# Optimization experiments

Hardware: AMD Instinct MI355X
Metric: run time of the kernel (lower is better)

## Reference

```python
import jax, jax.numpy as jnp
import numpy as np

B, D, H, N, K, C = 1024, 256, 512, 100000, 96, 10


def setup_inputs() -> dict:
    key = jax.random.key(0)
    ks = jax.random.split(key, 16)
    s = 0.02
    return {
        "x": jax.random.normal(ks[0], (B, D), jnp.float32),
        "candidate_x": jax.random.normal(ks[1], (N, D), jnp.float32),
        "candidate_labels": jax.random.randint(ks[2], (N,), 0, C, jnp.int32),
        "W_enc": jax.random.normal(ks[3], (D, H), jnp.float32) * s,
        "b_enc": jnp.zeros((H,), jnp.float32),
        "W_key": jax.random.normal(ks[4], (H, H), jnp.float32) * s,
        "b_key": jnp.zeros((H,), jnp.float32),
        "W_val": jax.random.normal(ks[5], (H, H), jnp.float32) * s,
        "b_val": jnp.zeros((H,), jnp.float32),
        "E_label": jax.random.normal(ks[6], (C, H), jnp.float32) * s,
        "W_t1": jax.random.normal(ks[7], (H, H), jnp.float32) * s,
        "b_t1": jnp.zeros((H,), jnp.float32),
        "W_t2": jax.random.normal(ks[8], (H, H), jnp.float32) * s,
    }


def reference(x, candidate_x, candidate_labels, W_enc, b_enc, W_key, b_key,
              W_val, b_val, E_label, W_t1, b_t1, W_t2):
    # Encode queries and candidates
    x_enc = x @ W_enc + b_enc                       # [B, H]
    cand_enc = candidate_x @ W_enc + b_enc          # [N, H]
    x_key = x_enc @ W_key + b_key                   # [B, H]
    cand_keys = cand_enc @ W_key + b_key            # [N, H]

    # Negative euclidean distance via GEMM expansion (compute-efficient cdist)
    q2 = jnp.sum(x_key * x_key, axis=-1, keepdims=True)        # [B, 1]
    c2 = jnp.sum(cand_keys * cand_keys, axis=-1)               # [N]
    d2 = q2 + c2[None, :] - 2.0 * (x_key @ cand_keys.T)        # [B, N]
    sim = -jnp.sqrt(jnp.maximum(d2, 0.0))                      # [B, N]

    # Top-k retrieval
    top_sims, top_idx = jax.lax.top_k(sim, K)                  # [B, K]

    cand_vals = cand_enc @ W_val + b_val                       # [N, H]
    label_emb = E_label[candidate_labels]                      # [N, H]

    ctx_keys = cand_keys[top_idx]                              # [B, K, H]
    ctx_labels = label_emb[top_idx]                            # [B, K, H]
    _ = cand_vals[top_idx]  # gathered values (unused by the original math)

    # Attention over retrieved context (softmax of top-k similarities)
    attn = jax.nn.softmax(top_sims, axis=1)                    # [B, K]

    # Correction MLP T (dropout is identity in eval mode)
    diff = x_key[:, None, :] - ctx_keys                        # [B, K, H]
    t_out = jax.nn.relu(diff @ W_t1 + b_t1) @ W_t2             # [B, K, H]

    ctx_vec = jnp.sum(attn[..., None] * (ctx_labels + t_out), axis=1)  # [B, H]
    return x_enc + ctx_vec
```

## Files before the change

### kernel.cpp

```cpp
#include <hip/hip_runtime.h>
#include <cfloat>
#include <cmath>

#define B_ 1024
#define D_ 256
#define H_ 512
#define N_ 100000
#define K_ 96
#define C_ 10
#define SAMP 8192
#define CAPC 4096
#define RCAP 15

typedef __attribute__((ext_vector_type(8))) short bf16x8;
typedef __attribute__((ext_vector_type(4))) float f32x4;

__device__ __forceinline__ float bf2f(ushort h) {
    union { unsigned u; float f; } v; v.u = ((unsigned)h) << 16; return v.f;
}
__device__ __forceinline__ ushort f2bf(float f) {
    union { float f; unsigned u; } v; v.f = f;
    unsigned u = v.u;
    unsigned r = (u + 0x7fffu + ((u >> 16) & 1u)) >> 16;
    return (ushort)r;
}
__device__ __forceinline__ unsigned f2key(float f) {
    unsigned u = __float_as_uint(f);
    return (u & 0x80000000u) ? ~u : (u | 0x80000000u);
}
__device__ __forceinline__ float d2_of(float acc, float q2, float c2) {
    return fmaxf(fmaf(-2.f, acc, q2 + c2), 0.f);
}

#define GLDS(g, l)                                                            \
    __builtin_amdgcn_global_load_lds(                                         \
        (const __attribute__((address_space(1))) void*)(g),                   \
        (__attribute__((address_space(3))) void*)(l), 16, 0, 0)

template <int RELU>
__global__ __launch_bounds__(256) void gemm_nn(const float* __restrict__ A,
                                               const float* __restrict__ Bm,
                                               const float* __restrict__ bias,
                                               float* __restrict__ Cm,
                                               int M, int N, int Kd) {
    __shared__ float sA[16][68];
    __shared__ float sB[16][64];
    const int t  = threadIdx.x;
    const int tx = t & 15, ty = t >> 4;
    const int m0 = blockIdx.y * 64;
    const int n0 = blockIdx.x * 64;
    const int lr = t >> 2;
    const int lk = (t & 3) << 2;
    const int bk = t >> 4;
    const int bn = (t & 15) << 2;

    float acc[4][4] = {};
    for (int k0 = 0; k0 < Kd; k0 += 16) {
        float4 av = make_float4(0.f, 0.f, 0.f, 0.f);
        if (m0 + lr < M)
            av = *(const float4*)(A + (size_t)(m0 + lr) * Kd + k0 + lk);
        sA[lk + 0][lr] = av.x; sA[lk + 1][lr] = av.y;
        sA[lk + 2][lr] = av.z; sA[lk + 3][lr] = av.w;
        float4 bv = *(const float4*)(Bm + (size_t)(k0 + bk) * N + n0 + bn);
        *(float4*)&sB[bk][bn] = bv;
        __syncthreads();
#pragma unroll
        for (int kk = 0; kk < 16; ++kk) {
            float4 a4 = *(const float4*)&sA[kk][ty << 2];
            float4 b4 = *(const float4*)&sB[kk][tx << 2];
            float ar[4] = {a4.x, a4.y, a4.z, a4.w};
            float br[4] = {b4.x, b4.y, b4.z, b4.w};
#pragma unroll
            for (int i = 0; i < 4; ++i)
#pragma unroll
                for (int j = 0; j < 4; ++j)
                    acc[i][j] = fmaf(ar[i], br[j], acc[i][j]);
        }
        __syncthreads();
    }
#pragma unroll
    for (int i = 0; i < 4; ++i) {
        int row = m0 + (ty << 2) + i;
        if (row < M) {
            int col = n0 + (tx << 2);
            float b0 = 0.f, b1 = 0.f, b2 = 0.f, b3 = 0.f;
            if (bias) { b0 = bias[col]; b1 = bias[col + 1]; b2 = bias[col + 2]; b3 = bias[col + 3]; }
            float4 o;
            o.x = acc[i][0] + b0; o.y = acc[i][1] + b1;
            o.z = acc[i][2] + b2; o.w = acc[i][3] + b3;
            if (RELU) {
                o.x = fmaxf(o.x, 0.f); o.y = fmaxf(o.y, 0.f);
                o.z = fmaxf(o.z, 0.f); o.w = fmaxf(o.w, 0.f);
            }
            *(float4*)(Cm + (size_t)row * N + col) = o;
        }
    }
}

template <int MODE, int SWZ>
__global__ __launch_bounds__(256) void gemm_nt(const ushort* __restrict__ A,
                                               const ushort* __restrict__ Bv,
                                               const float* __restrict__ bias,
                                               const float* __restrict__ q2v,
                                               const float* __restrict__ c2v,
                                               const float* __restrict__ thrv,
                                               float* __restrict__ candV,
                                               int* __restrict__ candI,
                                               int* __restrict__ cnt,
                                               void* __restrict__ Cout,
                                               int M, int Nlim, int K,
                                               int ldc, int nvalid, int per) {
    int m0, n0;
    if (SWZ == 0) {
        m0 = blockIdx.y * 128; n0 = blockIdx.x * 128;
    } else if (SWZ == 1) {
        int bid = blockIdx.x;
        int xcd = bid & 7, slot = bid >> 3;
        m0 = (slot & 7) * 128;
        n0 = (xcd * per + (slot >> 3)) * 128;
        if (n0 >= nvalid || m0 >= M) return;
    } else {
        int bid = blockIdx.x;
        int xcd = bid & 7, slot = bid >> 3;
        n0 = (slot & 3) * 128;
        m0 = (xcd * per + (slot >> 2)) * 128;
        if (m0 >= M) return;
    }

    __shared__ __align__(16) char smem[16896];
    ushort* sA = (ushort*)smem;
    ushort* sB = (ushort*)(smem + 8192);
    const int t = threadIdx.x;
    const int lane = t & 63, w = t >> 6;
    const int wm = w & 1, wn = w >> 1;

    f32x4 acc[4][4];
#pragma unroll
    for (int i = 0; i < 4; ++i)
#pragma unroll
        for (int j = 0; j < 4; ++j)
            acc[i][j] = (f32x4){0.f, 0.f, 0.f, 0.f};

    const int la = lane & 15, lk = lane >> 4;
    const int aoff = (wm * 64 + la) * 64 + lk * 16;
    const int boff = (wn * 64 + la) * 64 + lk * 16;
    const int r_ = t >> 2, cc_ = (t & 3);

    for (int k0 = 0; k0 < K; k0 += 32) {
#pragma unroll
        for (int q = 0; q < 2; ++q) {
            int r = r_ + q * 64;
            int ar = m0 + r; ar = (ar < M) ? ar : (M - 1);
            GLDS(A + (size_t)ar * K + k0 + cc_ * 8, (char*)sA + (q * 256 + t) * 16);
            int br = n0 + r; br = (br < Nlim) ? br : (Nlim - 1);
            GLDS(Bv + (size_t)br * K + k0 + cc_ * 8, (char*)sB + (q * 256 + t) * 16);
        }
        __syncthreads();
        bf16x8 af[4], bfr[4];
#pragma unroll
        for (int i = 0; i < 4; ++i)
            af[i] = *(const bf16x8*)((const char*)sA + aoff + i * 1024);
#pragma unroll
        for (int j = 0; j < 4; ++j)
            bfr[j] = *(const bf16x8*)((const char*)sB + boff + j * 1024);
#pragma unroll
        for (int i = 0; i < 4; ++i)
#pragma unroll
            for (int j = 0; j < 4; ++j)
                acc[i][j] = __builtin_amdgcn_mfma_f32_16x16x32_bf16(
                    af[i], bfr[j], acc[i][j], 0, 0, 0);
        __syncthreads();
    }

    const int rl = (lane >> 4) * 4, cl = lane & 15;

    if (MODE == 5) {
        float* stV = (float*)smem;
        int*   stI = (int*)(smem + 7680);
        int*   stC = (int*)(smem + 16384);
        for (int r = t; r < 128; r += 256) stC[r] = 0;
        __syncthreads();
#pragma unroll
        for (int i = 0; i < 4; ++i) {
#pragma unroll
            for (int v = 0; v < 4; ++v) {
                int rloc = wm * 64 + i * 16 + rl + v;
                int gr = m0 + rloc;
                float q2b = q2v[gr];
                float th = thrv[gr];
#pragma unroll
                for (int j = 0; j < 4; ++j) {
                    int gc = n0 + wn * 64 + j * 16 + cl;
                    if (gc < nvalid) {
                        float d2 = d2_of(acc[i][j][v], q2b, c2v[gc]);
                        if (d2 <= th) {
                            int p = atomicAdd(&stC[rloc], 1);
                            if (p < RCAP) {
                                stV[rloc * RCAP + p] = d2;
                                stI[rloc * RCAP + p] = gc;
                            }
                        }
                    }
                }
            }
        }
        __syncthreads();
        for (int r = t; r < 128; r += 256) {
            int n = stC[r]; if (n > RCAP) n = RCAP;
            if (n > 0) {
                int gr = m0 + r;
                int gb = atomicAdd(&cnt[gr], n);
                for (int q = 0; q < n; ++q) {
                    int pos = gb + q;
                    if (pos < CAPC) {
                        candV[(size_t)gr * CAPC + pos] = stV[r * RCAP + q];
                        candI[(size_t)gr * CAPC + pos] = stI[r * RCAP + q];
                    }
                }
            }
        }
        return;
    }

#pragma unroll
    for (int i = 0; i < 4; ++i) {
#pragma unroll
        for (int j = 0; j < 4; ++j) {
            int gc = n0 + wn * 64 + j * 16 + cl;
#pragma unroll
            for (int v = 0; v < 4; ++v) {
                int gr = m0 + wm * 64 + i * 16 + rl + v;
                if (gr < M && gc < nvalid) {
                    float val = acc[i][j][v];
                    if (MODE == 2) {
                        ((float*)Cout)[(size_t)gr * ldc + gc] = val;
                    } else {
                        if (MODE == 1 || MODE == 3) val += bias[gc];
                        if (MODE == 1) val = fmaxf(val, 0.f);
                        ((ushort*)Cout)[(size_t)gr * ldc + gc] = f2bf(val);
                    }
                }
            }
        }
    }
}

__global__ __launch_bounds__(256) void thr_select(const float* __restrict__ S,
                                                  int ld,
                                                  const float* __restrict__ q2v,
                                                  const float* __restrict__ c2v,
                                                  float* __restrict__ thrArr) {
    __shared__ unsigned keys[SAMP];
    __shared__ int hist[256];
    __shared__ int sel[2];
    const int b = blockIdx.x, t = threadIdx.x;
    const float q2b = q2v[b];
    for (int i = t; i < SAMP; i += 256)
        keys[i] = ~f2key(d2_of(S[(size_t)b * ld + i], q2b, c2v[i]));
    __syncthreads();
    unsigned prefix = 0, mask = 0;
    int rank = K_;
    for (int shift = 24; shift >= 0; shift -= 8) {
        hist[t & 255] = 0;
        __syncthreads();
        for (int i = t; i < SAMP; i += 256) {
            unsigned k = keys[i];
            if ((k & mask) == prefix) atomicAdd(&hist[(k >> shift) & 255], 1);
        }
        __syncthreads();
        if (t == 0) {
            int r = rank, d = 255;
            for (; d > 0; --d) { int c = hist[d]; if (r - c <= 0) break; r -= c; }
            sel[0] = d; sel[1] = (r < 1) ? 1 : r;
        }
        __syncthreads();
        prefix |= ((unsigned)sel[0]) << shift;
        rank = sel[1];
        mask |= (0xFFu << shift);
        __syncthreads();
    }
    if (t == 0) {
        unsigned key = ~prefix;
        thrArr[b] = __uint_as_float(key & 0x7FFFFFFFu);
    }
}

__global__ __launch_bounds__(256) void final_select(const float* __restrict__ candV,
                                                    const int* __restrict__ candI,
                                                    const int* __restrict__ cnt,
                                                    float* __restrict__ topV,
                                                    int* __restrict__ topI) {
    __shared__ unsigned keys[CAPC];
    __shared__ int hist[256];
    __shared__ int sel[2];
    __shared__ int poscnt, eqcnt;
    const int b = blockIdx.x, t = threadIdx.x;
    int n = cnt[b]; if (n > CAPC) n = CAPC;
    for (int i = t; i < n; i += 256)
        keys[i] = ~f2key(candV[(size_t)b * CAPC + i]);
    __syncthreads();
    unsigned prefix = 0, mask = 0;
    int rank = K_;
    for (int shift = 24; shift >= 0; shift -= 8) {
        hist[t & 255] = 0;
        __syncthreads();
        for (int i = t; i < n; i += 256) {
            unsigned k = keys[i];
            if ((k & mask) == prefix) atomicAdd(&hist[(k >> shift) & 255], 1);
        }
        __syncthreads();
        if (t == 0) {
            int r = rank, d = 255;
            for (; d > 0; --d) { int c = hist[d]; if (r - c <= 0) break; r -= c; }
            sel[0] = d; sel[1] = (r < 1) ? 1 : r;
        }
        __syncthreads();
        prefix |= ((unsigned)sel[0]) << shift;
        rank = sel[1];
        mask |= (0xFFu << shift);
        __syncthreads();
    }
    unsigned kth = prefix;
    if (t == 0) { poscnt = 0; eqcnt = 0; }
    __syncthreads();
    for (int i = t; i < n; i += 256) {
        if (keys[i] > kth) {
            int p = atomicAdd(&poscnt, 1);
            topV[b * K_ + p] = candV[(size_t)b * CAPC + i];
            topI[b * K_ + p] = candI[(size_t)b * CAPC + i];
        }
    }
    __syncthreads();
    int base = poscnt;
    for (int i = t; i < n; i += 256) {
        if (keys[i] == kth) {
            int p = atomicAdd(&eqcnt, 1);
            if (base + p < K_) {
                topV[b * K_ + base + p] = candV[(size_t)b * CAPC + i];
                topI[b * K_ + base + p] = candI[(size_t)b * CAPC + i];
            }
        }
    }
}

__global__ void init_cnt(int* cnt) {
    int i = blockIdx.x * 256 + threadIdx.x;
    if (i < B_) cnt[i] = 0;
}

__global__ void conv_f2b(const float* __restrict__ in, ushort* __restrict__ out, int n) {
    int i = (blockIdx.x * 256 + threadIdx.x) * 4;
    int stride = gridDim.x * 256 * 4;
    for (; i < n; i += stride) {
        float4 v = *(const float4*)(in + i);
        ushort4 o;
        o.x = f2bf(v.x); o.y = f2bf(v.y); o.z = f2bf(v.z); o.w = f2bf(v.w);
        *(ushort4*)(out + i) = o;
    }
}

__global__ __launch_bounds__(256) void transpose_f2b(const float* __restrict__ in,
                                                     ushort* __restrict__ out,
                                                     int R, int Cn) {
    __shared__ float tile[32][33];
    int bx = blockIdx.x * 32, by = blockIdx.y * 32;
    int tx = threadIdx.x & 31, ty = threadIdx.x >> 5;
    int x = bx + tx;
#pragma unroll
    for (int dy = 0; dy < 32; dy += 8) {
        int y = by + ty + dy;
        if (x < Cn && y < R) tile[ty + dy][tx] = in[(size_t)y * Cn + x];
    }
    __syncthreads();
    int ox = by + tx;
#pragma unroll
    for (int dy = 0; dy < 32; dy += 8) {
        int oy = bx + ty + dy;
        if (ox < R && oy < Cn) out[(size_t)oy * R + ox] = f2bf(tile[tx][ty + dy]);
    }
}

__global__ __launch_bounds__(64) void rowsq_b(const ushort* __restrict__ X,
                                              float* __restrict__ outv) {
    const int r = blockIdx.x, t = threadIdx.x;
    const ushort* p = X + (size_t)r * H_;
    ushort4 a = *(const ushort4*)(p + t * 4);
    ushort4 b = *(const ushort4*)(p + 256 + t * 4);
    float ax = bf2f(a.x), ay = bf2f(a.y), az = bf2f(a.z), aw = bf2f(a.w);
    float bx = bf2f(b.x), by = bf2f(b.y), bz = bf2f(b.z), bw = bf2f(b.w);
    float v = ax * ax + ay * ay + az * az + aw * aw +
              bx * bx + by * by + bz * bz + bw * bw;
    for (int off = 32; off > 0; off >>= 1) v += __shfl_down(v, off);
    if (t == 0) outv[r] = v;
}

__global__ void bcomb_k(const float* __restrict__ b_enc,
                        const float* __restrict__ W_key,
                        const float* __restrict__ b_key,
                        float* __restrict__ b_comb) {
    int h = blockIdx.x * 256 + threadIdx.x;
    if (h >= H_) return;
    float acc = b_key[h];
    for (int m = 0; m < H_; ++m)
        acc = fmaf(b_enc[m], W_key[(size_t)m * H_ + h], acc);
    b_comb[h] = acc;
}

__global__ __launch_bounds__(128) void softmax_k(const float* __restrict__ topVal,
                                                 float* __restrict__ attn) {
    __shared__ float red[128];
    const int b = blockIdx.x, t = threadIdx.x;
    float v = (t < K_) ? -sqrtf(topVal[b * K_ + t]) : -FLT_MAX;
    red[t] = v; __syncthreads();
    for (int s = 64; s > 0; s >>= 1) {
        if (t < s) red[t] = fmaxf(red[t], red[t + s]);
        __syncthreads();
    }
    float m = red[0]; __syncthreads();
    float e = (t < K_) ? expf(v - m) : 0.f;
    red[t] = e; __syncthreads();
    for (int s = 64; s > 0; s >>= 1) {
        if (t < s) red[t] += red[t + s];
        __syncthreads();
    }
    float ssum = red[0];
    if (t < K_) attn[b * K_ + t] = e / ssum;
}

__global__ __launch_bounds__(128) void gather_diff_b(const float* __restrict__ XK,
                                                     const ushort* __restrict__ CK,
                                                     const int* __restrict__ topI,
                                                     ushort* __restrict__ diff,
                                                     int b0) {
    const int r = blockIdx.x;
    const int b = b0 + r / K_;
    const int idx = topI[b * K_ + (r % K_)];
    const int t = threadIdx.x;
    float4 xv = *(const float4*)(XK + (size_t)b * H_ + t * 4);
    ushort4 cv = *(const ushort4*)(CK + (size_t)idx * H_ + t * 4);
    ushort4 o;
    o.x = f2bf(xv.x - bf2f(cv.x));
    o.y = f2bf(xv.y - bf2f(cv.y));
    o.z = f2bf(xv.z - bf2f(cv.z));
    o.w = f2bf(xv.w - bf2f(cv.w));
    *(ushort4*)(diff + (size_t)r * H_ + t * 4) = o;
}

__global__ __launch_bounds__(256) void wsum_h(const float* __restrict__ attn,
                                              const ushort* __restrict__ h,
                                              ushort* __restrict__ hw, int b0) {
    const int bl = blockIdx.x;
    const int b = b0 + bl;
    const int t = threadIdx.x;
    float a0 = 0.f, a1 = 0.f;
    const float* ap = attn + b * K_;
    for (int k = 0; k < K_; ++k) {
        float w = ap[k];
        const ushort* hr = h + (size_t)(bl * K_ + k) * H_;
        a0 = fmaf(w, bf2f(hr[t]), a0);
        a1 = fmaf(w, bf2f(hr[t + 256]), a1);
    }
    hw[(size_t)b * H_ + t]       = f2bf(a0);
    hw[(size_t)b * H_ + t + 256] = f2bf(a1);
}

__global__ __launch_bounds__(256) void final_out(const float* __restrict__ attn,
                                                 const int* __restrict__ topI,
                                                 const int* __restrict__ labels,
                                                 const float* __restrict__ E,
                                                 const float* __restrict__ tsum,
                                                 const float* __restrict__ xe,
                                                 float* __restrict__ out) {
    const int b = blockIdx.x, t = threadIdx.x;
    float a0 = 0.f, a1 = 0.f;
    for (int k = 0; k < K_; ++k) {
        float w = attn[b * K_ + k];
        int idx = topI[b * K_ + k];
        int lab = labels[idx];
        const float* el = E + (size_t)lab * H_;
        a0 = fmaf(w, el[t], a0);
        a1 = fmaf(w, el[t + 256], a1);
    }
    out[(size_t)b * H_ + t] =
        xe[(size_t)b * H_ + t] + a0 + tsum[(size_t)b * H_ + t];
    out[(size_t)b * H_ + t + 256] =
        xe[(size_t)b * H_ + t + 256] + a1 + tsum[(size_t)b * H_ + t + 256];
}

extern "C" void kernel_launch(void* const* d_in, const int* in_sizes, int n_in,
                              void* d_out, int out_size, void* d_ws, size_t ws_size,
                              hipStream_t stream) {
    const float* x      = (const float*)d_in[0];
    const float* cx     = (const float*)d_in[1];
    const int*   labels = (const int*)d_in[2];
    const float* W_enc  = (const float*)d_in[3];
    const float* b_enc  = (const float*)d_in[4];
    const float* W_key  = (const float*)d_in[5];
    const float* b_key  = (const float*)d_in[6];
    const float* E_label = (const float*)d_in[9];
    const float* W_t1   = (const float*)d_in[10];
    const float* b_t1   = (const float*)d_in[11];
    const float* W_t2   = (const float*)d_in[12];
    float* out = (float*)d_out;

    char* base = (char*)d_ws;
    size_t off = 0;
    auto take = [&](size_t n) -> char* {
        char* p = base + off;
        off = (off + n + 255) & ~(size_t)255;
        return p;
    };
    float*  Wc    = (float*)take((size_t)D_ * H_ * 4);
    float*  bc    = (float*)take((size_t)H_ * 4);
    ushort* WcT   = (ushort*)take((size_t)H_ * D_ * 2);
    ushort* Wt1T  = (ushort*)take((size_t)H_ * H_ * 2);
    ushort* Wt2T  = (ushort*)take((size_t)H_ * H_ * 2);
    float*  xe    = (float*)take((size_t)B_ * H_ * 4);
    float*  xk    = (float*)take((size_t)B_ * H_ * 4);
    ushort* xkb   = (ushort*)take((size_t)B_ * H_ * 2);
    float*  q2    = (float*)take((size_t)B_ * 4);
    ushort* ckb   = (ushort*)take((size_t)N_ * H_ * 2);
    float*  c2    = (float*)take((size_t)N_ * 4);
    float*  topV  = (float*)take((size_t)B_ * K_ * 4);
    int*    topI  = (int*)take((size_t)B_ * K_ * 4);
    float*  thr   = (float*)take((size_t)B_ * 4);
    float*  attn  = (float*)take((size_t)B_ * K_ * 4);
    int*    cnt   = (int*)take((size_t)B_ * 4);
    float*  candV = (float*)take((size_t)B_ * CAPC * 4);
    int*    candI = (int*)take((size_t)B_ * CAPC * 4);
    ushort* hwAll = (ushort*)take((size_t)B_ * H_ * 2);
    float*  tsum  = (float*)take((size_t)B_ * H_ * 4);
    char*   big   = base + off;
    size_t rem = (ws_size > off) ? (ws_size - off) : 0;

    ushort* cxb      = (ushort*)big;
    float*  simSmall = (float*)big;

    long long bcq = (long long)(rem / ((size_t)K_ * H_ * 2 * 2));
    if (bcq > B_) bcq = B_;
    if (bcq < 1) bcq = 1;
    int Bc = (int)bcq;

    {
        dim3 g(H_ / 64, D_ / 64);
        gemm_nn<0><<<g, 256, 0, stream>>>(W_enc, W_key, nullptr, Wc, D_, H_, H_);
        bcomb_k<<<(H_ + 255) / 256, 256, 0, stream>>>(b_enc, W_key, b_key, bc);
        dim3 gt1((H_ + 31) / 32, (D_ + 31) / 32);
        transpose_f2b<<<gt1, 256, 0, stream>>>(Wc, WcT, D_, H_);
        dim3 gt2((H_ + 31) / 32, (H_ + 31) / 32);
        transpose_f2b<<<gt2, 256, 0, stream>>>(W_t1, Wt1T, H_, H_);
        transpose_f2b<<<gt2, 256, 0, stream>>>(W_t2, Wt2T, H_, H_);
    }
    {
        dim3 gx(H_ / 64, B_ / 64);
        gemm_nn<0><<<gx, 256, 0, stream>>>(x, W_enc, b_enc, xe, B_, H_, D_);
        gemm_nn<0><<<gx, 256, 0, stream>>>(x, Wc, bc, xk, B_, H_, D_);
        conv_f2b<<<1024, 256, 0, stream>>>(xk, xkb, B_ * H_);
        conv_f2b<<<2048, 256, 0, stream>>>(cx, cxb, N_ * D_);
    }
    {
        int mt = (N_ + 127) / 128;
        int mper = (mt + 7) / 8;
        gemm_nt<3, 2><<<8 * mper * 4, 256, 0, stream>>>(
            cxb, WcT, bc, nullptr, nullptr, nullptr, nullptr, nullptr, nullptr,
            ckb, N_, H_, D_, H_, H_, mper);
    }
    rowsq_b<<<N_, 64, 0, stream>>>(ckb, c2);
    rowsq_b<<<B_, 64, 0, stream>>>(xkb, q2);

    {
        int nper = (SAMP / 128 + 7) / 8;
        gemm_nt<2, 1><<<64 * nper, 256, 0, stream>>>(
            xkb, ckb, nullptr, nullptr, nullptr, nullptr, nullptr, nullptr,
            nullptr, simSmall, B_, N_, H_, SAMP, SAMP, nper);
        thr_select<<<B_, 256, 0, stream>>>(simSmall, SAMP, q2, c2, thr);
    }
    init_cnt<<<(B_ + 255) / 256, 256, 0, stream>>>(cnt);
    {
        int NT = (N_ + 127) / 128;
        int nper = (NT + 7) / 8;
        gemm_nt<5, 1><<<64 * nper, 256, 0, stream>>>(
            xkb, ckb, nullptr, q2, c2, thr, candV, candI, cnt,
            nullptr, B_, N_, H_, 0, N_, nper);
    }
    final_select<<<B_, 256, 0, stream>>>(candV, candI, cnt, topV, topI);
    softmax_k<<<B_, 128, 0, stream>>>(topV, attn);

    ushort* diffB = (ushort*)big;
    ushort* hB = (ushort*)(big + (size_t)Bc * K_ * H_ * 2);
    for (int b0 = 0; b0 < B_; b0 += Bc) {
        int bcn = min(Bc, B_ - b0);
        int Mrows = bcn * K_;
        gather_diff_b<<<Mrows, 128, 0, stream>>>(xk, ckb, topI, diffB, b0);
        int mt4 = (Mrows + 127) / 128;
        int mper4 = (mt4 + 7) / 8;
        gemm_nt<1, 2><<<8 * mper4 * 4, 256, 0, stream>>>(
            diffB, Wt1T, b_t1, nullptr, nullptr, nullptr, nullptr, nullptr,
            nullptr, hB, Mrows, H_, H_, H_, H_, mper4);
        wsum_h<<<bcn, 256, 0, stream>>>(attn, hB, hwAll, b0);
    }
    {
        dim3 g(H_ / 128, B_ / 128);
        gemm_nt<2, 0><<<g, 256, 0, stream>>>(
            hwAll, Wt2T, nullptr, nullptr, nullptr, nullptr, nullptr, nullptr,
            nullptr, tsum, B_, H_, H_, H_, H_, 0);
    }
    final_out<<<B_, 256, 0, stream>>>(attn, topI, labels, E_label, tsum, xe, out);
}
```

Measured before the change: 968.9 us.

## Add 256x256-tile 8-wave GEMM with ping-pong LDS pipeline for large GEMMs

Introduces a new gemm256 kernel that uses 256x256 output tiles with 512 threads, double-buffered global-to-LDS staging, and interleaved MFMA/LDS-read phases with explicit barriers and priority hints. It replaces the 128-tile gemm_nt in the candidate-key projection, the fused distance/threshold-filter GEMM, and the correction-MLP first layer. Larger tiles raise arithmetic intensity and data reuse per workgroup, and the filter epilogue now stages survivors per row in a larger shared buffer before writing them out globally. The cost is higher register and LDS use (128KB shared), possible occupancy loss, and tile-quantisation waste on ragged M.

```diff
diff --git a/kernel.cpp b/kernel.cpp
--- a/kernel.cpp
+++ b/kernel.cpp
@@ -11,6 +11,7 @@
 #define SAMP 8192
 #define CAPC 4096
 #define RCAP 15
+#define RCAP2 24
 
 typedef __attribute__((ext_vector_type(8))) short bf16x8;
 typedef __attribute__((ext_vector_type(4))) float f32x4;
@@ -243,6 +244,219 @@
             }
         }
     }
+}
+
+#define FENCE() asm volatile("" ::: "memory")
+#define PBAR()                                                                \
+    { FENCE(); __builtin_amdgcn_s_barrier();                                  \
+      asm volatile("s_waitcnt lgkmcnt(0)" ::: "memory"); }
+#define PBARV4()                                                              \
+    { asm volatile("s_waitcnt vmcnt(4)" ::: "memory");                        \
+      __builtin_amdgcn_s_barrier(); FENCE(); }
+#define BAR2()                                                                \
+    { FENCE(); __builtin_amdgcn_s_barrier(); FENCE(); }
+
+template <int MODE, int MMINOR>
+__global__ __launch_bounds__(512, 2) void gemm256(
+    const ushort* __restrict__ A, const ushort* __restrict__ Bv,
+    const float* __restrict__ bias, const float* __restrict__ q2v,
+    const float* __restrict__ c2v, const float* __restrict__ thrv,
+    float* __restrict__ candV, int* __restrict__ candI, int* __restrict__ cnt,
+    void* __restrict__ Cout, int M, int Nlim, int K, int ldc, int nvalid) {
+    __shared__ __align__(16) char smem[131072];
+
+    const int nwg = gridDim.x;
+    const int MT = (M + 255) >> 8;
+    const int q8 = nwg >> 3, r8 = nwg & 7;
+    const int xcd = blockIdx.x & 7, lin = blockIdx.x >> 3;
+    const int wgid =
+        (xcd < r8 ? xcd * (q8 + 1) : r8 * (q8 + 1) + (xcd - r8) * q8) + lin;
+    int mt, nt;
+    if (MMINOR) { mt = wgid % MT; nt = wgid / MT; }
+    else        { int NT = nwg / MT; nt = wgid % NT; mt = wgid / NT; }
+    const int m0 = mt << 8, n0 = nt << 8;
+
+    const int t = threadIdx.x;
+    const int lane = t & 63, w = t >> 6;
+    const int wm = w & 1, wn = w >> 1;
+    const int la = lane & 15, lk = lane >> 4;
+    const int e7 = la & 7;
+    const int gk0 = (lk ^ e7) << 4;
+    const int gk1 = ((4 | lk) ^ e7) << 4;
+
+    char* sA = smem;
+    char* sB = smem + 65536;
+    const int rbA = wm * 16384 + la * 128;
+    const int rbB = (wn >> 1) * 16384 + ((wn & 1) * 64 + la) * 128;
+
+    const int g8   = (((t & 7) ^ ((t >> 3) & 7)) << 3);
+    const int srow = t >> 3;
+    const int sdst = t * 16;
+
+    auto stageA = [&](int kt, int buf) {
+        const ushort* p = A + kt * 64 + g8;
+        char* d = sA + buf * 32768;
+#pragma unroll
+        for (int h = 0; h < 2; ++h)
+#pragma unroll
+            for (int qq = 0; qq < 2; ++qq) {
+                int row = m0 + h * 128 + qq * 64 + srow;
+                row = (row < M) ? row : (M - 1);
+                GLDS(p + (size_t)row * K, d + h * 16384 + qq * 8192 + sdst);
+            }
+    };
+    auto stageB = [&](int kt, int buf) {
+        const ushort* p = Bv + kt * 64 + g8;
+        char* d = sB + buf * 32768;
+#pragma unroll
+        for (int h = 0; h < 2; ++h)
+#pragma unroll
+            for (int qq = 0; qq < 2; ++qq) {
+                int row = n0 + h * 128 + qq * 64 + srow;
+                row = (row < Nlim) ? row : (Nlim - 1);
+                GLDS(p + (size_t)row * K, d + h * 16384 + qq * 8192 + sdst);
+            }
+    };
+    auto ldA4 = [&](int buf, int qq, int gk, bf16x8* dst) {
+        const char* pb = sA + buf * 32768 + rbA + qq * 8192 + gk;
+#pragma unroll
+        for (int mf = 0; mf < 4; ++mf)
+            dst[mf] = *(const bf16x8*)(pb + mf * 2048);
+    };
+    auto ldB4 = [&](int buf, int gk, bf16x8* dst) {
+        const char* pb = sB + buf * 32768 + rbB + gk;
+#pragma unroll
+        for (int nf = 0; nf < 4; ++nf)
+            dst[nf] = *(const bf16x8*)(pb + nf * 2048);
+    };
+
+    f32x4 acc[2][4][4];
+#pragma unroll
+    for (int i = 0; i < 2; ++i)
+#pragma unroll
+        for (int j = 0; j < 4; ++j)
+#pragma unroll
+            for (int k = 0; k < 4; ++k)
+                acc[i][j][k] = (f32x4){0.f, 0.f, 0.f, 0.f};
+
+    auto mfma16 = [&](f32x4 (*ac)[4], const bf16x8* a, const bf16x8* b) {
+        __builtin_amdgcn_s_setprio(1);
+#pragma unroll
+        for (int mf = 0; mf < 4; ++mf)
+#pragma unroll
+            for (int nf = 0; nf < 4; ++nf)
+                ac[mf][nf] = __builtin_amdgcn_mfma_f32_16x16x32_bf16(
+                    a[mf], b[nf], ac[mf][nf], 0, 0, 0);
+        __builtin_amdgcn_s_setprio(0);
+    };
+
+    bf16x8 aX[4], aY[4], bb0[4], bb1[4];
+    const int NK = K >> 6;
+
+    stageA(0, 0); stageB(0, 0); stageA(1, 1);
+    asm volatile("s_waitcnt vmcnt(4)" ::: "memory");
+    __builtin_amdgcn_s_barrier(); FENCE();
+
+    for (int it = 0; it < (NK >> 1); ++it) {
+        const int k2 = it * 2;
+        const int kA2 = (k2 + 2 < NK) ? k2 + 2 : NK - 1;
+        const int kA3 = (k2 + 3 < NK) ? k2 + 3 : NK - 1;
+        ldA4(0, 0, gk0, aX); ldB4(0, gk0, bb0);
+        stageB(k2 + 1, 1);
+        PBAR(); mfma16(acc[0], aX, bb0); BAR2();
+        ldA4(0, 1, gk0, aY); ldB4(0, gk1, bb1);
+        PBAR(); mfma16(acc[1], aY, bb0); BAR2();
+        ldA4(0, 0, gk1, aX); ldA4(0, 1, gk1, aY);
+        PBAR(); mfma16(acc[0], aX, bb1); BAR2();
+        stageA(kA2, 0);
+        PBARV4(); mfma16(acc[1], aY, bb1); BAR2();
+        ldA4(1, 0, gk0, aX); ldB4(1, gk0, bb0);
+        stageB(kA2, 0);
+        PBAR(); mfma16(acc[0], aX, bb0); BAR2();
+        ldA4(1, 1, gk0, aY); ldB4(1, gk1, bb1);
+        PBAR(); mfma16(acc[1], aY, bb0); BAR2();
+        ldA4(1, 0, gk1, aX); ldA4(1, 1, gk1, aY);
+        PBAR(); mfma16(acc[0], aX, bb1); BAR2();
+        stageA(kA3, 1);
+        PBARV4(); mfma16(acc[1], aY, bb1); BAR2();
+    }
+    asm volatile("s_waitcnt vmcnt(0)" ::: "memory");
+    __builtin_amdgcn_s_barrier();
+
+    const int rl = lk * 4, cl = la;
+
+    if (MODE == 5) {
+        float* stV = (float*)smem;
+        int*   stI = (int*)(smem + 256 * RCAP2 * 4);
+        int*   stC = (int*)(smem + 256 * RCAP2 * 8);
+        for (int r = t; r < 256; r += 512) stC[r] = 0;
+        __syncthreads();
+#pragma unroll
+        for (int qq = 0; qq < 2; ++qq)
+#pragma unroll
+            for (int mf = 0; mf < 4; ++mf) {
+#pragma unroll
+                for (int v = 0; v < 4; ++v) {
+                    int rloc = wm * 128 + qq * 64 + mf * 16 + rl + v;
+                    int gr = m0 + rloc;
+                    float q2b = q2v[gr];
+                    float th = thrv[gr];
+#pragma unroll
+                    for (int nf = 0; nf < 4; ++nf) {
+                        int gc = n0 + wn * 64 + nf * 16 + cl;
+                        if (gc < nvalid) {
+                            float d2 = d2_of(acc[qq][mf][nf][v], q2b, c2v[gc]);
+                            if (d2 <= th) {
+                                int p = atomicAdd(&stC[rloc], 1);
+                                if (p < RCAP2) {
+                                    stV[rloc * RCAP2 + p] = d2;
+                                    stI[rloc * RCAP2 + p] = gc;
+                                }
+                            }
+                        }
+                    }
+                }
+            }
+        __syncthreads();
+        for (int r = t; r < 256; r += 512) {
+            int n = stC[r]; if (n > RCAP2) n = RCAP2;
+            if (n > 0) {
+                int gr = m0 + r;
+                int gb = atomicAdd(&cnt[gr], n);
+                for (int qi = 0; qi < n; ++qi) {
+                    int pos = gb + qi;
+                    if (pos < CAPC) {
+                        candV[(size_t)gr * CAPC + pos] = stV[r * RCAP2 + qi];
+                        candI[(size_t)gr * CAPC + pos] = stI[r * RCAP2 + qi];
+                    }
+                }
+            }
+        }
+        return;
+    }
+
+#pragma unroll
+    for (int qq = 0; qq < 2; ++qq)
+#pragma unroll
+        for (int mf = 0; mf < 4; ++mf)
+#pragma unroll
+            for (int nf = 0; nf < 4; ++nf) {
+                int gc = n0 + wn * 64 + nf * 16 + cl;
+#pragma unroll
+                for (int v = 0; v < 4; ++v) {
+                    int gr = m0 + wm * 128 + qq * 64 + mf * 16 + rl + v;
+                    if (gr < M && gc < nvalid) {
+                        float val = acc[qq][mf][nf][v];
+                        if (MODE == 2) {
+                            ((float*)Cout)[(size_t)gr * ldc + gc] = val;
+                        } else {
+                            if (MODE == 1 || MODE == 3) val += bias[gc];
+                            if (MODE == 1) val = fmaxf(val, 0.f);
+                            ((ushort*)Cout)[(size_t)gr * ldc + gc] = f2bf(val);
+                        }
+                    }
+                }
+            }
 }
 
 __global__ __launch_bounds__(256) void thr_select(const float* __restrict__ S,
@@ -559,11 +773,10 @@
         conv_f2b<<<2048, 256, 0, stream>>>(cx, cxb, N_ * D_);
     }
     {
-        int mt = (N_ + 127) / 128;
-        int mper = (mt + 7) / 8;
-        gemm_nt<3, 2><<<8 * mper * 4, 256, 0, stream>>>(
+        int MT = (N_ + 255) / 256;
+        gemm256<3, 0><<<MT * 2, 512, 0, stream>>>(
             cxb, WcT, bc, nullptr, nullptr, nullptr, nullptr, nullptr, nullptr,
-            ckb, N_, H_, D_, H_, H_, mper);
+            ckb, N_, H_, D_, H_, H_);
     }
     rowsq_b<<<N_, 64, 0, stream>>>(ckb, c2);
     rowsq_b<<<B_, 64, 0, stream>>>(xkb, q2);
@@ -577,11 +790,10 @@
     }
     init_cnt<<<(B_ + 255) / 256, 256, 0, stream>>>(cnt);
     {
-        int NT = (N_ + 127) / 128;
-        int nper = (NT + 7) / 8;
-        gemm_nt<5, 1><<<64 * nper, 256, 0, stream>>>(
+        int NT = (N_ + 255) / 256;
+        gemm256<5, 1><<<4 * NT, 512, 0, stream>>>(
             xkb, ckb, nullptr, q2, c2, thr, candV, candI, cnt,
-            nullptr, B_, N_, H_, 0, N_, nper);
+            nullptr, B_, N_, H_, 0, N_);
     }
     final_select<<<B_, 256, 0, stream>>>(candV, candI, cnt, topV, topI);
     softmax_k<<<B_, 128, 0, stream>>>(topV, attn);
@@ -592,11 +804,10 @@
         int bcn = min(Bc, B_ - b0);
         int Mrows = bcn * K_;
         gather_diff_b<<<Mrows, 128, 0, stream>>>(xk, ckb, topI, diffB, b0);
-        int mt4 = (Mrows + 127) / 128;
-        int mper4 = (mt4 + 7) / 8;
-        gemm_nt<1, 2><<<8 * mper4 * 4, 256, 0, stream>>>(
+        int mt4 = (Mrows + 255) / 256;
+        gemm256<1, 0><<<mt4 * 2, 512, 0, stream>>>(
             diffB, Wt1T, b_t1, nullptr, nullptr, nullptr, nullptr, nullptr,
-            nullptr, hB, Mrows, H_, H_, H_, H_, mper4);
+            nullptr, hB, Mrows, H_, H_, H_, H_);
         wsum_h<<<bcn, 256, 0, stream>>>(attn, hB, hwAll, b0);
     }
     {
```

Result: no change. 987.9 us (+2.0%).

## Compute query-candidate distances in input space via projected queries

Applied to the files above, without the earlier changes.

Rewrites the distance GEMM algebraically: instead of x_key·cand_keys over H=512, it projects the queries through the combined encoder-key weights (xk·Wc^T, giving a 256-wide vector) and dots them with the raw bf16 candidate inputs over D=256. The candidate bias term is folded into a per-query correction, q2x = |xk|^2 - 2·xk·bc. This halves the reduction depth of the two big B×N GEMMs (threshold sampling and the full filter pass). The change also halves the threshold sample size, reuses the candV buffer for the sample scores, and adds a global-atomic spill path for rows whose per-block shared staging overflows. The risk is extra bf16 rounding in the projected queries, which could alter which neighbours land near the top-k boundary, and a smaller sample gives a looser threshold with more candidates.

```diff
diff --git a/kernel.cpp b/kernel.cpp
--- a/kernel.cpp
+++ b/kernel.cpp
@@ -8,7 +8,7 @@
 #define N_ 100000
 #define K_ 96
 #define C_ 10
-#define SAMP 8192
+#define SAMP 4096
 #define CAPC 4096
 #define RCAP 15
 
@@ -198,6 +198,12 @@
                             if (p < RCAP) {
                                 stV[rloc * RCAP + p] = d2;
                                 stI[rloc * RCAP + p] = gc;
+                            } else {
+                                int gp = atomicAdd(&cnt[gr], 1);
+                                if (gp < CAPC) {
+                                    candV[(size_t)gr * CAPC + gp] = d2;
+                                    candI[(size_t)gr * CAPC + gp] = gc;
+                                }
                             }
                         }
                     }
@@ -394,6 +400,27 @@
     if (t == 0) outv[r] = v;
 }
 
+__global__ __launch_bounds__(64) void q2x_k(const ushort* __restrict__ Xb,
+                                            const float* __restrict__ Xf,
+                                            const float* __restrict__ bc,
+                                            float* __restrict__ outv) {
+    const int r = blockIdx.x, t = threadIdx.x;
+    const ushort* p  = Xb + (size_t)r * H_ + t * 8;
+    const float*  xf = Xf + (size_t)r * H_ + t * 8;
+    float nrm = 0.f, dot = 0.f;
+#pragma unroll
+    for (int j = 0; j < 8; ++j) {
+        float v = bf2f(p[j]);
+        nrm = fmaf(v, v, nrm);
+        dot = fmaf(xf[j], bc[t * 8 + j], dot);
+    }
+    for (int off = 32; off > 0; off >>= 1) {
+        nrm += __shfl_down(nrm, off);
+        dot += __shfl_down(dot, off);
+    }
+    if (t == 0) outv[r] = nrm - 2.f * dot;
+}
+
 __global__ void bcomb_k(const float* __restrict__ b_enc,
                         const float* __restrict__ W_key,
                         const float* __restrict__ b_key,
@@ -513,12 +540,14 @@
     float*  Wc    = (float*)take((size_t)D_ * H_ * 4);
     float*  bc    = (float*)take((size_t)H_ * 4);
     ushort* WcT   = (ushort*)take((size_t)H_ * D_ * 2);
+    ushort* Wcb   = (ushort*)take((size_t)D_ * H_ * 2);
     ushort* Wt1T  = (ushort*)take((size_t)H_ * H_ * 2);
     ushort* Wt2T  = (ushort*)take((size_t)H_ * H_ * 2);
     float*  xe    = (float*)take((size_t)B_ * H_ * 4);
     float*  xk    = (float*)take((size_t)B_ * H_ * 4);
     ushort* xkb   = (ushort*)take((size_t)B_ * H_ * 2);
-    float*  q2    = (float*)take((size_t)B_ * 4);
+    ushort* xprojb= (ushort*)take((size_t)B_ * D_ * 2);
+    float*  q2x   = (float*)take((size_t)B_ * 4);
     ushort* ckb   = (ushort*)take((size_t)N_ * H_ * 2);
     float*  c2    = (float*)take((size_t)N_ * 4);
     float*  topV  = (float*)take((size_t)B_ * K_ * 4);
@@ -533,8 +562,8 @@
     char*   big   = base + off;
     size_t rem = (ws_size > off) ? (ws_size - off) : 0;
 
-    ushort* cxb      = (ushort*)big;
-    float*  simSmall = (float*)big;
+    ushort* cxb = (ushort*)big;
+    float* simSmall = (float*)candV;
 
     long long bcq = (long long)(rem / ((size_t)K_ * H_ * 2 * 2));
     if (bcq > B_) bcq = B_;
@@ -547,6 +576,7 @@
         bcomb_k<<<(H_ + 255) / 256, 256, 0, stream>>>(b_enc, W_key, b_key, bc);
         dim3 gt1((H_ + 31) / 32, (D_ + 31) / 32);
         transpose_f2b<<<gt1, 256, 0, stream>>>(Wc, WcT, D_, H_);
+        conv_f2b<<<128, 256, 0, stream>>>(Wc, Wcb, D_ * H_);
         dim3 gt2((H_ + 31) / 32, (H_ + 31) / 32);
         transpose_f2b<<<gt2, 256, 0, stream>>>(W_t1, Wt1T, H_, H_);
         transpose_f2b<<<gt2, 256, 0, stream>>>(W_t2, Wt2T, H_, H_);
@@ -557,6 +587,11 @@
         gemm_nn<0><<<gx, 256, 0, stream>>>(x, Wc, bc, xk, B_, H_, D_);
         conv_f2b<<<1024, 256, 0, stream>>>(xk, xkb, B_ * H_);
         conv_f2b<<<2048, 256, 0, stream>>>(cx, cxb, N_ * D_);
+        dim3 gp(D_ / 128, B_ / 128);
+        gemm_nt<0, 0><<<gp, 256, 0, stream>>>(
+            xkb, Wcb, nullptr, nullptr, nullptr, nullptr, nullptr, nullptr,
+            nullptr, xprojb, B_, D_, H_, D_, D_, 0);
+        q2x_k<<<B_, 64, 0, stream>>>(xkb, xk, bc, q2x);
     }
     {
         int mt = (N_ + 127) / 128;
@@ -566,22 +601,21 @@
             ckb, N_, H_, D_, H_, H_, mper);
     }
     rowsq_b<<<N_, 64, 0, stream>>>(ckb, c2);
-    rowsq_b<<<B_, 64, 0, stream>>>(xkb, q2);
 
     {
         int nper = (SAMP / 128 + 7) / 8;
         gemm_nt<2, 1><<<64 * nper, 256, 0, stream>>>(
-            xkb, ckb, nullptr, nullptr, nullptr, nullptr, nullptr, nullptr,
-            nullptr, simSmall, B_, N_, H_, SAMP, SAMP, nper);
-        thr_select<<<B_, 256, 0, stream>>>(simSmall, SAMP, q2, c2, thr);
+            xprojb, cxb, nullptr, nullptr, nullptr, nullptr, nullptr, nullptr,
+            nullptr, simSmall, B_, N_, D_, SAMP, SAMP, nper);
+        thr_select<<<B_, 256, 0, stream>>>(simSmall, SAMP, q2x, c2, thr);
     }
     init_cnt<<<(B_ + 255) / 256, 256, 0, stream>>>(cnt);
     {
         int NT = (N_ + 127) / 128;
         int nper = (NT + 7) / 8;
         gemm_nt<5, 1><<<64 * nper, 256, 0, stream>>>(
-            xkb, ckb, nullptr, q2, c2, thr, candV, candI, cnt,
-            nullptr, B_, N_, H_, 0, N_, nper);
+            xprojb, cxb, nullptr, q2x, c2, thr, candV, candI, cnt,
+            nullptr, B_, N_, D_, 0, N_, nper);
     }
     final_select<<<B_, 256, 0, stream>>>(candV, candI, cnt, topV, topI);
     softmax_k<<<B_, 128, 0, stream>>>(topV, attn);
```

Result: faster. 929.3 us (-4.1%).
